# Performance work log

Hardware: AMD Instinct MI355X
Metric: run time of the kernel (lower is better)

Reference implementation:

```python
import jax, jax.numpy as jnp
import numpy as np

N = 128  # n_hidden == n_inputs == n_outputs
TWO_PI = 2.0 * np.pi


def build_unitary(mzi_phases, output_phases):
    """Clements mesh: n layers of disjoint 2x2 MZI rotations, composed left-to-right.
    Within a layer the MZIs act on disjoint pairs, so their product equals one dense
    layer matrix (matches the sequential torch loop exactly)."""
    n = N
    U = jnp.eye(n, dtype=jnp.complex64)
    idx = 0
    for layer in range(n):
        pi = np.arange(layer % 2, n - 1, 2)  # left indices of pairs this layer
        m = len(pi)
        theta = mzi_phases[idx:idx + 2 * m:2]
        phi = mzi_phases[idx + 1:idx + 2 * m:2]
        idx += 2 * m
        ct = jnp.cos(theta).astype(jnp.complex64)
        st = jnp.sin(theta).astype(jnp.complex64)
        ep = jnp.exp(1j * phi.astype(jnp.complex64))
        L = jnp.eye(n, dtype=jnp.complex64)
        L = L.at[pi, pi].set(ct * ep)
        L = L.at[pi, pi + 1].set(st)
        L = L.at[pi + 1, pi].set(st)
        L = L.at[pi + 1, pi + 1].set(-ct * jnp.conj(ep))
        U = U @ L
    return U * jnp.exp(1j * output_phases.astype(jnp.complex64))[None, :]


def nofu(z, alpha, beta):
    eps = 1e-8
    intensity = jnp.abs(z) ** 2 + eps
    a = jnp.clip(alpha, 0.0, 10.0)
    b = jnp.clip(beta, 0.0, 10.0)
    transmission = jnp.exp(-a[None, :] / (1.0 + b[None, :] * intensity))
    return z * jnp.sqrt(transmission).astype(z.dtype)


def setup_inputs() -> dict:
    key = jax.random.key(0)
    ks = jax.random.split(key, 16)
    B = 65536
    num_mzi_phases = N * (N - 1)  # 2 phases per MZI
    inp = {
        "x": jax.random.normal(ks[0], (B, N), jnp.float32),
        "input_phases": jnp.zeros((N,), jnp.float32),
        "mzi_phases1": jax.random.uniform(ks[1], (num_mzi_phases,), jnp.float32) * TWO_PI,
        "out_phases1": jnp.zeros((N,), jnp.float32),
        "alpha1": jnp.full((N,), 0.5, jnp.float32),
        "beta1": jnp.full((N,), 0.2, jnp.float32),
        "mzi_phases2": jax.random.uniform(ks[2], (num_mzi_phases,), jnp.float32) * TWO_PI,
        "out_phases2": jnp.zeros((N,), jnp.float32),
        "alpha2": jnp.full((N,), 0.5, jnp.float32),
        "beta2": jnp.full((N,), 0.2, jnp.float32),
        "mzi_phases3": jax.random.uniform(ks[3], (num_mzi_phases,), jnp.float32) * TWO_PI,
        "out_phases3": jnp.zeros((N,), jnp.float32),
        "W": jax.random.normal(ks[4], (N, 2 * N), jnp.float32) * 0.05,  # torch Linear weight [out,in]
        "b": jnp.zeros((N,), jnp.float32),
    }
    return inp


def reference(x, input_phases, mzi_phases1, out_phases1, alpha1, beta1,
              mzi_phases2, out_phases2, alpha2, beta2,
              mzi_phases3, out_phases3, W, b):
    # Eval mode: no BatchNorm, no dropout.
    z = x.astype(jnp.complex64) * jnp.exp(1j * input_phases.astype(jnp.complex64))[None, :]
    z = z @ build_unitary(mzi_phases1, out_phases1)
    z = nofu(z, alpha1, beta1)
    z = z @ build_unitary(mzi_phases2, out_phases2)
    z = nofu(z, alpha2, beta2)
    z = z @ build_unitary(mzi_phases3, out_phases3)
    real_output = jnp.concatenate([jnp.real(z), jnp.imag(z)], axis=1)
    return real_output @ W.T + b[None, :]
```

## Files before the change

### kernel.cpp

```cpp
#include <hip/hip_runtime.h>
#include <math.h>

typedef __attribute__((ext_vector_type(8))) short bf16x8;
typedef __attribute__((ext_vector_type(4))) float f32x4;
typedef unsigned short u16;

__device__ __forceinline__ unsigned short f2bf(float f) {
    unsigned u = __builtin_bit_cast(unsigned, f);
    u += 0x7fffu + ((u >> 16) & 1u);
    return (unsigned short)(u >> 16);
}

__global__ __launch_bounds__(128) void prep_all_kernel(
    const float* __restrict__ mzi1, const float* __restrict__ mzi2,
    const float* __restrict__ mzi3, const float* __restrict__ inph,
    const float* __restrict__ outph1, const float* __restrict__ outph2,
    const float* __restrict__ outph3, const float* __restrict__ W,
    u16* __restrict__ P1, u16* __restrict__ P2, u16* __restrict__ P3,
    u16* __restrict__ P4)
{
    const int b = blockIdx.x, t = threadIdx.x;

    if (b >= 384) {
        const int n = b - 384;
        const int j = t;
        const int rre = ((j >> 4) * 32) + (j & 15);
        P4[n * 256 + rre]      = f2bf(W[n * 256 + j]);
        P4[n * 256 + rre + 16] = f2bf(W[n * 256 + j + 128]);
        return;
    }
    if (t >= 64) return;

    const int s = b >> 7, r = b & 127;
    const float* mzi = (s == 0) ? mzi1 : ((s == 1) ? mzi2 : mzi3);

    float2 a = make_float2(0.f, 0.f), b2 = make_float2(0.f, 0.f);
    if (s == 0) {
        float sp, cp; __sincosf(inph[r], &sp, &cp);
        if (2 * t == r)     a  = make_float2(cp, sp);
        if (2 * t + 1 == r) b2 = make_float2(cp, sp);
    } else {
        if (2 * t == r)     a.x  = 1.f;
        if (2 * t + 1 == r) b2.x = 1.f;
    }

    auto ldmz = [&](int L) -> float2 {
        const int start = L & 1;
        const int m = 64 - start;
        if (t < m) {
            const int off = (L >> 1) * 254 + start * 128 + 2 * t;
            return *(const float2*)(mzi + off);
        }
        return make_float2(0.f, 0.f);
    };
    float2 mz[4];
    #pragma unroll
    for (int i = 0; i < 4; ++i) mz[i] = ldmz(i);

    #pragma unroll 4
    for (int L = 0; L < 128; ++L) {
        const float2 v = mz[L & 3];
        if (L < 124) mz[L & 3] = ldmz(L + 4);
        float st, ct, sp, cp;
        __sincosf(v.x, &st, &ct);
        __sincosf(v.y, &sp, &cp);
        if ((L & 1) == 0) {
            float pr = ct * (a.x * cp - a.y * sp) + st * b2.x;
            float pi = ct * (a.x * sp + a.y * cp) + st * b2.y;
            float qr = st * a.x - ct * (b2.x * cp + b2.y * sp);
            float qi = st * a.y - ct * (b2.y * cp - b2.x * sp);
            a = make_float2(pr, pi); b2 = make_float2(qr, qi);
        } else {
            float2 an;
            an.x = __shfl_down(a.x, 1); an.y = __shfl_down(a.y, 1);
            float pr = ct * (b2.x * cp - b2.y * sp) + st * an.x;
            float pi = ct * (b2.x * sp + b2.y * cp) + st * an.y;
            float qr = st * b2.x - ct * (an.x * cp + an.y * sp);
            float qi = st * b2.y - ct * (an.y * cp - an.x * sp);
            if (t < 63) b2 = make_float2(pr, pi);
            float2 qs;
            qs.x = __shfl_up(qr, 1); qs.y = __shfl_up(qi, 1);
            if (t >= 1) a = qs;
        }
    }

    const float* outph = (s == 0) ? outph1 : ((s == 1) ? outph2 : outph3);
    #pragma unroll
    for (int h = 0; h < 2; ++h) {
        const int j = 2 * t + h;
        float2 w = h ? b2 : a;
        float sp, cp; __sincosf(outph[j], &sp, &cp);
        const float wr = w.x * cp - w.y * sp;
        const float wi = w.x * sp + w.y * cp;
        const int cre = ((j >> 4) * 32) + (j & 15);
        if (s == 0) {
            P1[cre * 128 + r]        = f2bf(wr);
            P1[(cre + 16) * 128 + r] = f2bf(wi);
        } else {
            u16* P = (s == 1) ? P2 : P3;
            const int rre = ((r >> 4) * 32) + (r & 15);
            P[cre * 256 + rre]             = f2bf(wr);
            P[cre * 256 + rre + 16]        = f2bf(-wi);
            P[(cre + 16) * 256 + rre]      = f2bf(wi);
            P[(cre + 16) * 256 + rre + 16] = f2bf(wr);
        }
    }
}

__global__ __launch_bounds__(512, 4) void ficonn_mfma_kernel(
    const float* __restrict__ x,
    const u16* __restrict__ P1, const u16* __restrict__ P2,
    const u16* __restrict__ P3, const u16* __restrict__ P4,
    const float* __restrict__ al1, const float* __restrict__ be1,
    const float* __restrict__ al2, const float* __restrict__ be2,
    const float* __restrict__ bias, float* __restrict__ out)
{
    __shared__ __align__(16) char zBuf[2][32768];
    char* const z0 = zBuf[0];
    char* const z1 = zBuf[1];

    const int tid  = threadIdx.x;
    const int lane = tid & 63;
    const int wv   = tid >> 6;
    const int l16  = lane & 15;
    const int kg   = lane >> 4;
    const int nb   = wv * 32;
    const size_t rowBase = (size_t)blockIdx.x * 64;

    const int jf = wv * 16 + l16;
    const float av1 = 0.5f * fminf(fmaxf(al1[jf], 0.f), 10.f);
    const float bv1 = fminf(fmaxf(be1[jf], 0.f), 10.f);
    const float av2 = 0.5f * fminf(fmaxf(al2[jf], 0.f), 10.f);
    const float bv2 = fminf(fmaxf(be2[jf], 0.f), 10.f);

    {
        const float4* xg = (const float4*)(x + rowBase * 128);
        #pragma unroll
        for (int i = 0; i < 4; ++i) {
            const int idx = tid + i * 512;
            const int row = idx >> 5;
            const int c4  = idx & 31;
            float4 f = xg[idx];
            uint2 v;
            v.x = (unsigned)f2bf(f.x) | ((unsigned)f2bf(f.y) << 16);
            v.y = (unsigned)f2bf(f.z) | ((unsigned)f2bf(f.w) << 16);
            const unsigned byte = ((unsigned)(row * 512 + c4 * 8)) ^ ((unsigned)(row & 31) << 4);
            *(uint2*)(z0 + byte) = v;
        }
    }
    __syncthreads();

    f32x4 acc[4][2];

    #pragma unroll
    for (int mt = 0; mt < 4; ++mt)
        #pragma unroll
        for (int nt = 0; nt < 2; ++nt) acc[mt][nt] = (f32x4){0.f, 0.f, 0.f, 0.f};

    #pragma unroll 2
    for (int ksl = 0; ksl < 4; ++ksl) {
        const int k0 = ksl * 32 + kg * 8;
        bf16x8 A[4];
        #pragma unroll
        for (int mt = 0; mt < 4; ++mt) {
            const int row = mt * 16 + l16;
            const unsigned byte = ((unsigned)(row * 512 + k0 * 2)) ^ ((unsigned)(row & 31) << 4);
            A[mt] = *(const bf16x8*)(z0 + byte);
        }
        #pragma unroll
        for (int nt = 0; nt < 2; ++nt) {
            bf16x8 Bf = *(const bf16x8*)&P1[(nb + nt * 16 + l16) * 128 + k0];
            #pragma unroll
            for (int mt = 0; mt < 4; ++mt)
                acc[mt][nt] = __builtin_amdgcn_mfma_f32_16x16x32_bf16(A[mt], Bf, acc[mt][nt], 0, 0, 0);
        }
    }

    #pragma unroll
    for (int mt = 0; mt < 4; ++mt)
        #pragma unroll
        for (int r = 0; r < 4; ++r) {
            float re = acc[mt][0][r], im = acc[mt][1][r];
            float I = fmaf(re, re, fmaf(im, im, 1e-8f));
            float fct = __expf(__fdividef(-av1, fmaf(bv1, I, 1.f)));
            re *= fct; im *= fct;
            const int row = mt * 16 + kg * 4 + r;
            const int colRe = nb + l16;
            const unsigned sw = (unsigned)(row & 31) << 4;
            *(u16*)(z1 + (((unsigned)(row * 512 + colRe * 2)) ^ sw)) = f2bf(re);
            *(u16*)(z1 + (((unsigned)(row * 512 + (colRe + 16) * 2)) ^ sw)) = f2bf(im);
        }
    __syncthreads();

    #pragma unroll
    for (int mt = 0; mt < 4; ++mt)
        #pragma unroll
        for (int nt = 0; nt < 2; ++nt) acc[mt][nt] = (f32x4){0.f, 0.f, 0.f, 0.f};

    #pragma unroll 2
    for (int ks = 0; ks < 8; ++ks) {
        const int k0 = ks * 32 + kg * 8;
        bf16x8 A[4];
        #pragma unroll
        for (int mt = 0; mt < 4; ++mt) {
            const int row = mt * 16 + l16;
            const unsigned byte = ((unsigned)(row * 512 + k0 * 2)) ^ ((unsigned)(row & 31) << 4);
            A[mt] = *(const bf16x8*)(z1 + byte);
        }
        #pragma unroll
        for (int nt = 0; nt < 2; ++nt) {
            bf16x8 Bf = *(const bf16x8*)&P2[(nb + nt * 16 + l16) * 256 + k0];
            #pragma unroll
            for (int mt = 0; mt < 4; ++mt)
                acc[mt][nt] = __builtin_amdgcn_mfma_f32_16x16x32_bf16(A[mt], Bf, acc[mt][nt], 0, 0, 0);
        }
    }

    #pragma unroll
    for (int mt = 0; mt < 4; ++mt)
        #pragma unroll
        for (int r = 0; r < 4; ++r) {
            float re = acc[mt][0][r], im = acc[mt][1][r];
            float I = fmaf(re, re, fmaf(im, im, 1e-8f));
            float fct = __expf(__fdividef(-av2, fmaf(bv2, I, 1.f)));
            re *= fct; im *= fct;
            const int row = mt * 16 + kg * 4 + r;
            const int colRe = nb + l16;
            const unsigned sw = (unsigned)(row & 31) << 4;
            *(u16*)(z0 + (((unsigned)(row * 512 + colRe * 2)) ^ sw)) = f2bf(re);
            *(u16*)(z0 + (((unsigned)(row * 512 + (colRe + 16) * 2)) ^ sw)) = f2bf(im);
        }
    __syncthreads();

    #pragma unroll
    for (int mt = 0; mt < 4; ++mt)
        #pragma unroll
        for (int nt = 0; nt < 2; ++nt) acc[mt][nt] = (f32x4){0.f, 0.f, 0.f, 0.f};

    #pragma unroll 2
    for (int ks = 0; ks < 8; ++ks) {
        const int k0 = ks * 32 + kg * 8;
        bf16x8 A[4];
        #pragma unroll
        for (int mt = 0; mt < 4; ++mt) {
            const int row = mt * 16 + l16;
            const unsigned byte = ((unsigned)(row * 512 + k0 * 2)) ^ ((unsigned)(row & 31) << 4);
            A[mt] = *(const bf16x8*)(z0 + byte);
        }
        #pragma unroll
        for (int nt = 0; nt < 2; ++nt) {
            bf16x8 Bf = *(const bf16x8*)&P3[(nb + nt * 16 + l16) * 256 + k0];
            #pragma unroll
            for (int mt = 0; mt < 4; ++mt)
                acc[mt][nt] = __builtin_amdgcn_mfma_f32_16x16x32_bf16(A[mt], Bf, acc[mt][nt], 0, 0, 0);
        }
    }

    #pragma unroll
    for (int mt = 0; mt < 4; ++mt)
        #pragma unroll
        for (int r = 0; r < 4; ++r) {
            const int row = mt * 16 + kg * 4 + r;
            const int colRe = nb + l16;
            const unsigned sw = (unsigned)(row & 31) << 4;
            *(u16*)(z1 + (((unsigned)(row * 512 + colRe * 2)) ^ sw)) = f2bf(acc[mt][0][r]);
            *(u16*)(z1 + (((unsigned)(row * 512 + (colRe + 16) * 2)) ^ sw)) = f2bf(acc[mt][1][r]);
        }
    __syncthreads();

    f32x4 facc[4];
    #pragma unroll
    for (int mt = 0; mt < 4; ++mt) facc[mt] = (f32x4){0.f, 0.f, 0.f, 0.f};

    const int nb2 = wv * 16;
    #pragma unroll 2
    for (int ks = 0; ks < 8; ++ks) {
        const int k0 = ks * 32 + kg * 8;
        bf16x8 A[4];
        #pragma unroll
        for (int mt = 0; mt < 4; ++mt) {
            const int row = mt * 16 + l16;
            const unsigned byte = ((unsigned)(row * 512 + k0 * 2)) ^ ((unsigned)(row & 31) << 4);
            A[mt] = *(const bf16x8*)(z1 + byte);
        }
        bf16x8 Bf = *(const bf16x8*)&P4[(nb2 + l16) * 256 + k0];
        #pragma unroll
        for (int mt = 0; mt < 4; ++mt)
            facc[mt] = __builtin_amdgcn_mfma_f32_16x16x32_bf16(A[mt], Bf, facc[mt], 0, 0, 0);
    }

    const float bcol = bias[nb2 + l16];
    #pragma unroll
    for (int mt = 0; mt < 4; ++mt)
        #pragma unroll
        for (int r = 0; r < 4; ++r) {
            const size_t row = rowBase + mt * 16 + kg * 4 + r;
            out[row * 128 + nb2 + l16] = facc[mt][r] + bcol;
        }
}

extern "C" void kernel_launch(void* const* d_in, const int* in_sizes, int n_in,
                              void* d_out, int out_size, void* d_ws, size_t ws_size,
                              hipStream_t stream)
{
    const float* x      = (const float*)d_in[0];
    const float* inph   = (const float*)d_in[1];
    const float* mzi1   = (const float*)d_in[2];
    const float* outph1 = (const float*)d_in[3];
    const float* alpha1 = (const float*)d_in[4];
    const float* beta1  = (const float*)d_in[5];
    const float* mzi2   = (const float*)d_in[6];
    const float* outph2 = (const float*)d_in[7];
    const float* alpha2 = (const float*)d_in[8];
    const float* beta2  = (const float*)d_in[9];
    const float* mzi3   = (const float*)d_in[10];
    const float* outph3 = (const float*)d_in[11];
    const float* W      = (const float*)d_in[12];
    const float* bias   = (const float*)d_in[13];

    const int B = in_sizes[0] / 128;

    u16* P1 = (u16*)d_ws;
    u16* P2 = P1 + 32768;
    u16* P3 = P2 + 65536;
    u16* P4 = P3 + 65536;

    prep_all_kernel<<<512, 128, 0, stream>>>(
        mzi1, mzi2, mzi3, inph, outph1, outph2, outph3, W, P1, P2, P3, P4);
    ficonn_mfma_kernel<<<B / 64, 512, 0, stream>>>(
        x, P1, P2, P3, P4, alpha1, beta1, alpha2, beta2, bias, (float*)d_out);
}
```

Before: 82.75 us.

## Fold third unitary into final linear weight via precombined matrix

```diff
diff --git a/kernel.cpp b/kernel.cpp
--- a/kernel.cpp
+++ b/kernel.cpp
@@ -10,25 +10,18 @@
     u += 0x7fffu + ((u >> 16) & 1u);
     return (unsigned short)(u >> 16);
 }
+__device__ __forceinline__ float bf2f(unsigned short v) {
+    return __builtin_bit_cast(float, (unsigned)v << 16);
+}
 
 __global__ __launch_bounds__(128) void prep_all_kernel(
     const float* __restrict__ mzi1, const float* __restrict__ mzi2,
     const float* __restrict__ mzi3, const float* __restrict__ inph,
     const float* __restrict__ outph1, const float* __restrict__ outph2,
-    const float* __restrict__ outph3, const float* __restrict__ W,
-    u16* __restrict__ P1, u16* __restrict__ P2, u16* __restrict__ P3,
-    u16* __restrict__ P4)
+    const float* __restrict__ outph3,
+    u16* __restrict__ P1, u16* __restrict__ P2, u16* __restrict__ P3)
 {
     const int b = blockIdx.x, t = threadIdx.x;
-
-    if (b >= 384) {
-        const int n = b - 384;
-        const int j = t;
-        const int rre = ((j >> 4) * 32) + (j & 15);
-        P4[n * 256 + rre]      = f2bf(W[n * 256 + j]);
-        P4[n * 256 + rre + 16] = f2bf(W[n * 256 + j + 128]);
-        return;
-    }
     if (t >= 64) return;
 
     const int s = b >> 7, r = b & 127;
@@ -107,10 +100,26 @@
     }
 }
 
+__global__ __launch_bounds__(256) void combine_kernel(
+    const u16* __restrict__ P3, const float* __restrict__ W,
+    u16* __restrict__ P34)
+{
+    const int n = blockIdx.x;
+    const int k = threadIdx.x;
+    float acc = 0.f;
+    #pragma unroll 4
+    for (int c = 0; c < 256; ++c) {
+        const int g = c >> 5, i = c & 31;
+        const int j = (i < 16) ? (g * 16 + i) : (128 + g * 16 + (i - 16));
+        acc = fmaf(bf2f(P3[c * 256 + k]), W[n * 256 + j], acc);
+    }
+    P34[n * 256 + k] = f2bf(acc);
+}
+
 __global__ __launch_bounds__(512, 4) void ficonn_mfma_kernel(
     const float* __restrict__ x,
     const u16* __restrict__ P1, const u16* __restrict__ P2,
-    const u16* __restrict__ P3, const u16* __restrict__ P4,
+    const u16* __restrict__ P34,
     const float* __restrict__ al1, const float* __restrict__ be1,
     const float* __restrict__ al2, const float* __restrict__ be2,
     const float* __restrict__ bias, float* __restrict__ out)
@@ -232,42 +241,6 @@
         }
     __syncthreads();
 
-    #pragma unroll
-    for (int mt = 0; mt < 4; ++mt)
-        #pragma unroll
-        for (int nt = 0; nt < 2; ++nt) acc[mt][nt] = (f32x4){0.f, 0.f, 0.f, 0.f};
-
-    #pragma unroll 2
-    for (int ks = 0; ks < 8; ++ks) {
-        const int k0 = ks * 32 + kg * 8;
-        bf16x8 A[4];
-        #pragma unroll
-        for (int mt = 0; mt < 4; ++mt) {
-            const int row = mt * 16 + l16;
-            const unsigned byte = ((unsigned)(row * 512 + k0 * 2)) ^ ((unsigned)(row & 31) << 4);
-            A[mt] = *(const bf16x8*)(z0 + byte);
-        }
-        #pragma unroll
-        for (int nt = 0; nt < 2; ++nt) {
-            bf16x8 Bf = *(const bf16x8*)&P3[(nb + nt * 16 + l16) * 256 + k0];
-            #pragma unroll
-            for (int mt = 0; mt < 4; ++mt)
-                acc[mt][nt] = __builtin_amdgcn_mfma_f32_16x16x32_bf16(A[mt], Bf, acc[mt][nt], 0, 0, 0);
-        }
-    }
-
-    #pragma unroll
-    for (int mt = 0; mt < 4; ++mt)
-        #pragma unroll
-        for (int r = 0; r < 4; ++r) {
-            const int row = mt * 16 + kg * 4 + r;
-            const int colRe = nb + l16;
-            const unsigned sw = (unsigned)(row & 31) << 4;
-            *(u16*)(z1 + (((unsigned)(row * 512 + colRe * 2)) ^ sw)) = f2bf(acc[mt][0][r]);
-            *(u16*)(z1 + (((unsigned)(row * 512 + (colRe + 16) * 2)) ^ sw)) = f2bf(acc[mt][1][r]);
-        }
-    __syncthreads();
-
     f32x4 facc[4];
     #pragma unroll
     for (int mt = 0; mt < 4; ++mt) facc[mt] = (f32x4){0.f, 0.f, 0.f, 0.f};
@@ -281,9 +254,9 @@
         for (int mt = 0; mt < 4; ++mt) {
             const int row = mt * 16 + l16;
             const unsigned byte = ((unsigned)(row * 512 + k0 * 2)) ^ ((unsigned)(row & 31) << 4);
-            A[mt] = *(const bf16x8*)(z1 + byte);
-        }
-        bf16x8 Bf = *(const bf16x8*)&P4[(nb2 + l16) * 256 + k0];
+            A[mt] = *(const bf16x8*)(z0 + byte);
+        }
+        bf16x8 Bf = *(const bf16x8*)&P34[(nb2 + l16) * 256 + k0];
         #pragma unroll
         for (int mt = 0; mt < 4; ++mt)
             facc[mt] = __builtin_amdgcn_mfma_f32_16x16x32_bf16(A[mt], Bf, facc[mt], 0, 0, 0);
@@ -320,13 +293,14 @@
 
     const int B = in_sizes[0] / 128;
 
-    u16* P1 = (u16*)d_ws;
-    u16* P2 = P1 + 32768;
-    u16* P3 = P2 + 65536;
-    u16* P4 = P3 + 65536;
-
-    prep_all_kernel<<<512, 128, 0, stream>>>(
-        mzi1, mzi2, mzi3, inph, outph1, outph2, outph3, W, P1, P2, P3, P4);
+    u16* P1  = (u16*)d_ws;
+    u16* P2  = P1 + 32768;
+    u16* P3  = P2 + 65536;
+    u16* P34 = P3 + 65536;
+
+    prep_all_kernel<<<384, 128, 0, stream>>>(
+        mzi1, mzi2, mzi3, inph, outph1, outph2, outph3, P1, P2, P3);
+    combine_kernel<<<128, 256, 0, stream>>>(P3, W, P34);
     ficonn_mfma_kernel<<<B / 64, 512, 0, stream>>>(
-        x, P1, P2, P3, P4, alpha1, beta1, alpha2, beta2, bias, (float*)d_out);
-}
+        x, P1, P2, P34, alpha1, beta1, alpha2, beta2, bias, (float*)d_out);
+}
```

After: 87.52 us. 5.8% more time.
